# Optimization experiments

Hardware: AMD Instinct MI355X
Metric: run time of the kernel (lower is better)

## Reference

```python
import jax, jax.numpy as jnp
import numpy as np

B, C, H, W = 8, 256, 160, 160

def setup_inputs() -> dict:
    key = jax.random.key(0)
    kx, kw, kh = jax.random.split(key, 3)
    x = jax.random.normal(kx, (B, C, H, W), dtype=jnp.float32)
    # kaiming_normal fan_in, relu -> std = sqrt(2/fan_in)
    fcw_w = jax.random.normal(kw, (1, W), dtype=jnp.float32) * np.float32(np.sqrt(2.0 / W))
    fch_w = jax.random.normal(kh, (1, H), dtype=jnp.float32) * np.float32(np.sqrt(2.0 / H))
    fcw_b = jnp.zeros((1,), dtype=jnp.float32)
    fch_b = jnp.zeros((1,), dtype=jnp.float32)
    return {"x": x, "fcw_w": fcw_w, "fcw_b": fcw_b, "fch_w": fch_w, "fch_b": fch_b}

def reference(x, fcw_w, fcw_b, fch_w, fch_b):
    b, c, h, w = x.shape
    xr = x.reshape(b * c, h, w)                                   # (n,h,w)
    # fc_w: Linear(w,1) then softmax over h (dim=1 of (n,h,1))
    alpha = jax.nn.softmax(jnp.einsum('nhw,w->nh', xr, fcw_w[0]) + fcw_b[0], axis=1)  # (n,h)
    # repeat+bmm == broadcasting a softmax-weighted row-sum to every row:
    # x_c[n,i,:] = sum_h alpha[n,h] * x[n,h,:]  (same for all i)
    row = jnp.einsum('nh,nhw->nw', alpha, xr)                      # (n,w)
    # fc_h on x_c^T (n,w,h): each h-column of x_c^T equals row, so the
    # Linear(h,1) reduces to row * sum(fch_w) + bias (identical math)
    beta = jax.nn.softmax(row * jnp.sum(fch_w[0]) + fch_b[0], axis=1)  # (n,w)
    # second repeat+bmm collapses to a scalar per (b,c): sum_w beta*row
    s = jnp.einsum('nw,nw->n', beta, row)                          # (n,)
    out = jnp.broadcast_to(s[:, None, None], (b * c, h, w)).reshape(b, c, h, w)
    return out
```

## Files before the change

### kernel.cpp

```cpp
#include <hip/hip_runtime.h>


#define HH 160
#define WW 160
#define NPLANE (HH * WW)
#define NPLANES 2048
#define NROWS (NPLANES * HH)

__global__ void __launch_bounds__(256) sa1_logits(
    const float* __restrict__ x,
    const float* __restrict__ fcw_w,
    float* __restrict__ l)
{
    const int wid  = (blockIdx.x * 256 + threadIdx.x) >> 6;
    const int lane = threadIdx.x & 63;

    float4 ww = make_float4(0.f, 0.f, 0.f, 0.f);
    if (lane < 40) ww = *(const float4*)(fcw_w + 4 * lane);

#pragma unroll 4
    for (int k = 0; k < 40; ++k) {
        const int r = wid + (k << 13);
        float p = 0.f;
        if (lane < 40) {
            const float4 xv = *(const float4*)(x + (size_t)r * WW + 4 * lane);
            p = xv.x * ww.x + xv.y * ww.y + xv.z * ww.z + xv.w * ww.w;
        }
#pragma unroll
        for (int off = 32; off >= 1; off >>= 1)
            p += __shfl_xor(p, off, 64);
        if (lane == 0) l[r] = p;
    }
}

__global__ void __launch_bounds__(256) sa1_attn(
    const float* __restrict__ x,
    const float* __restrict__ fch_w,
    const float* __restrict__ l,
    float* __restrict__ s_out)
{
    const int n    = blockIdx.x;
    const int t    = threadIdx.x;
    const int lane = t & 63;
    const int wv   = t >> 6;

    __shared__ float albuf[HH];
    __shared__ float pmax[4], psum[4], pS[4], pzb[4], psd[4];

    float lv = -1e30f, fv = 0.f;
    if (t < HH) { lv = l[n * HH + t]; fv = fch_w[t]; }
    float m = lv, fs = fv;
#pragma unroll
    for (int off = 32; off >= 1; off >>= 1) {
        m  = fmaxf(m, __shfl_xor(m, off, 64));
        fs += __shfl_xor(fs, off, 64);
    }
    if (lane == 0) { pmax[wv] = m; pS[wv] = fs; }
    __syncthreads();
    m = fmaxf(fmaxf(pmax[0], pmax[1]), fmaxf(pmax[2], pmax[3]));
    const float S = pS[0] + pS[1] + pS[2] + pS[3];

    float e = 0.f;
    if (t < HH) { e = __expf(lv - m); albuf[t] = e; }
    float zs = e;
#pragma unroll
    for (int off = 32; off >= 1; off >>= 1)
        zs += __shfl_xor(zs, off, 64);
    if (lane == 0) psum[wv] = zs;
    __syncthreads();
    const float Z = psum[0] + psum[1] + psum[2] + psum[3];

    float acc0 = 0.f, acc1 = 0.f, acc2 = 0.f, acc3 = 0.f;
    if (t < WW) {
        const float* xp = x + (size_t)n * NPLANE + t;
#pragma unroll 4
        for (int h = 0; h < HH; h += 4) {
            acc0 += albuf[h + 0] * xp[(h + 0) * WW];
            acc1 += albuf[h + 1] * xp[(h + 1) * WW];
            acc2 += albuf[h + 2] * xp[(h + 2) * WW];
            acc3 += albuf[h + 3] * xp[(h + 3) * WW];
        }
    }
    const float row = ((acc0 + acc1) + (acc2 + acc3)) / Z;

    float bl = (t < WW) ? row * S : -1e30f;
    float mb = bl;
#pragma unroll
    for (int off = 32; off >= 1; off >>= 1)
        mb = fmaxf(mb, __shfl_xor(mb, off, 64));
    if (lane == 0) pmax[wv] = mb;
    __syncthreads();
    mb = fmaxf(fmaxf(pmax[0], pmax[1]), fmaxf(pmax[2], pmax[3]));

    float e2 = (t < WW) ? __expf(bl - mb) : 0.f;
    float zb = e2, sd = e2 * row;
#pragma unroll
    for (int off = 32; off >= 1; off >>= 1) {
        zb += __shfl_xor(zb, off, 64);
        sd += __shfl_xor(sd, off, 64);
    }
    if (lane == 0) { pzb[wv] = zb; psd[wv] = sd; }
    __syncthreads();
    if (t == 0) {
        const float ZB = pzb[0] + pzb[1] + pzb[2] + pzb[3];
        const float SD = psd[0] + psd[1] + psd[2] + psd[3];
        s_out[n] = SD / ZB;
    }
}

__global__ void __launch_bounds__(256) sa1_bcast(
    const float* __restrict__ s_arr,
    float* __restrict__ out)
{
    const int n = blockIdx.x;
    const int t = threadIdx.x;
    float* op = out + (size_t)n * NPLANE;

    const float sv = s_arr[n];
    const float4 o = make_float4(sv, sv, sv, sv);
#pragma unroll
    for (int k = 0; k < 25; ++k)
        *(float4*)(op + 4 * (size_t)(k * 256 + t)) = o;
}

extern "C" void kernel_launch(void* const* d_in, const int* in_sizes, int n_in,
                              void* d_out, int out_size, void* d_ws, size_t ws_size,
                              hipStream_t stream) {
    const float* x     = (const float*)d_in[0];
    const float* fcw_w = (const float*)d_in[1];
    const float* fch_w = (const float*)d_in[3];
    float* out = (float*)d_out;

    float* l_ws = (float*)d_ws;
    float* s_ws = l_ws + NROWS;

    sa1_logits<<<NPLANES, 256, 0, stream>>>(x, fcw_w, l_ws);
    sa1_attn  <<<NPLANES, 256, 0, stream>>>(x, fch_w, l_ws, s_ws);
    sa1_bcast <<<NPLANES, 256, 0, stream>>>(s_ws, out);
}
```

Measured before the change: 393.6 us.

## Fuse logits and attention into one pass with online softmax

Merges the logits kernel and the attention kernel into a single kernel that reads each plane of x once. Each wave walks every fourth row, computes the row logit, and keeps an online-softmax running max, normaliser and weighted row accumulator. The four per-wave partials are then merged through shared memory. This removes the second full read of x and the intermediate logits buffer, at the cost of extra exp work per row and a serial dependency chain in each wave, with a one-row-ahead prefetch to hide load latency.

```diff
diff --git a/kernel.cpp b/kernel.cpp
--- a/kernel.cpp
+++ b/kernel.cpp
@@ -5,38 +5,11 @@
 #define WW 160
 #define NPLANE (HH * WW)
 #define NPLANES 2048
-#define NROWS (NPLANES * HH)
 
-__global__ void __launch_bounds__(256) sa1_logits(
+__global__ void __launch_bounds__(256, 8) sa1_reduce(
     const float* __restrict__ x,
     const float* __restrict__ fcw_w,
-    float* __restrict__ l)
-{
-    const int wid  = (blockIdx.x * 256 + threadIdx.x) >> 6;
-    const int lane = threadIdx.x & 63;
-
-    float4 ww = make_float4(0.f, 0.f, 0.f, 0.f);
-    if (lane < 40) ww = *(const float4*)(fcw_w + 4 * lane);
-
-#pragma unroll 4
-    for (int k = 0; k < 40; ++k) {
-        const int r = wid + (k << 13);
-        float p = 0.f;
-        if (lane < 40) {
-            const float4 xv = *(const float4*)(x + (size_t)r * WW + 4 * lane);
-            p = xv.x * ww.x + xv.y * ww.y + xv.z * ww.z + xv.w * ww.w;
-        }
-#pragma unroll
-        for (int off = 32; off >= 1; off >>= 1)
-            p += __shfl_xor(p, off, 64);
-        if (lane == 0) l[r] = p;
-    }
-}
-
-__global__ void __launch_bounds__(256) sa1_attn(
-    const float* __restrict__ x,
     const float* __restrict__ fch_w,
-    const float* __restrict__ l,
     float* __restrict__ s_out)
 {
     const int n    = blockIdx.x;
@@ -44,66 +17,85 @@
     const int lane = t & 63;
     const int wv   = t >> 6;
 
-    __shared__ float albuf[HH];
-    __shared__ float pmax[4], psum[4], pS[4], pzb[4], psd[4];
+    __shared__ float racc_s[4 * WW];
+    __shared__ float mzbuf[8];
+    __shared__ float pS[4];
+    __shared__ float red[12];
 
-    float lv = -1e30f, fv = 0.f;
-    if (t < HH) { lv = l[n * HH + t]; fv = fch_w[t]; }
-    float m = lv, fs = fv;
+    float fs = (t < HH) ? fch_w[t] : 0.f;
 #pragma unroll
-    for (int off = 32; off >= 1; off >>= 1) {
-        m  = fmaxf(m, __shfl_xor(m, off, 64));
-        fs += __shfl_xor(fs, off, 64);
+    for (int off = 32; off >= 1; off >>= 1) fs += __shfl_xor(fs, off, 64);
+    if (lane == 0) pS[wv] = fs;
+
+    float4 ww = make_float4(0.f, 0.f, 0.f, 0.f);
+    if (lane < 40) ww = *(const float4*)(fcw_w + 4 * lane);
+
+    const float* xp = x + (size_t)n * NPLANE;
+
+    float  m = -1e30f, Z = 0.f;
+    float4 racc = make_float4(0.f, 0.f, 0.f, 0.f);
+    float4 xv_next = make_float4(0.f, 0.f, 0.f, 0.f);
+    if (lane < 40) xv_next = *(const float4*)(xp + (size_t)wv * WW + 4 * lane);
+
+    for (int r = 0; r < 40; ++r) {
+        const float4 xv = xv_next;
+        if (r < 39 && lane < 40)
+            xv_next = *(const float4*)(xp + (size_t)(wv + 4 * (r + 1)) * WW + 4 * lane);
+
+        float p = (lane < 40)
+                    ? (xv.x * ww.x + xv.y * ww.y + xv.z * ww.z + xv.w * ww.w)
+                    : 0.f;
+#pragma unroll
+        for (int off = 32; off >= 1; off >>= 1) p += __shfl_xor(p, off, 64);
+        const float mn = fmaxf(m, p);
+        const float c  = __expf(m - mn);
+        const float e  = __expf(p - mn);
+        Z = Z * c + e;
+        racc.x = racc.x * c + e * xv.x;
+        racc.y = racc.y * c + e * xv.y;
+        racc.z = racc.z * c + e * xv.z;
+        racc.w = racc.w * c + e * xv.w;
+        m = mn;
     }
-    if (lane == 0) { pmax[wv] = m; pS[wv] = fs; }
+
+    if (lane < 40) *(float4*)(racc_s + wv * WW + 4 * lane) = racc;
+    if (lane == 0) { mzbuf[2 * wv] = m; mzbuf[2 * wv + 1] = Z; }
     __syncthreads();
-    m = fmaxf(fmaxf(pmax[0], pmax[1]), fmaxf(pmax[2], pmax[3]));
+
     const float S = pS[0] + pS[1] + pS[2] + pS[3];
+    const float m0 = mzbuf[0], m1 = mzbuf[2], m2 = mzbuf[4], m3 = mzbuf[6];
+    const float M  = fmaxf(fmaxf(m0, m1), fmaxf(m2, m3));
+    const float s0 = __expf(m0 - M), s1 = __expf(m1 - M);
+    const float s2 = __expf(m2 - M), s3 = __expf(m3 - M);
+    const float Zt = s0 * mzbuf[1] + s1 * mzbuf[3] + s2 * mzbuf[5] + s3 * mzbuf[7];
 
-    float e = 0.f;
-    if (t < HH) { e = __expf(lv - m); albuf[t] = e; }
-    float zs = e;
-#pragma unroll
-    for (int off = 32; off >= 1; off >>= 1)
-        zs += __shfl_xor(zs, off, 64);
-    if (lane == 0) psum[wv] = zs;
-    __syncthreads();
-    const float Z = psum[0] + psum[1] + psum[2] + psum[3];
+    float row = 0.f;
+    if (t < WW) {
+        const float rs = s0 * racc_s[0 * WW + t] + s1 * racc_s[1 * WW + t]
+                       + s2 * racc_s[2 * WW + t] + s3 * racc_s[3 * WW + t];
+        row = rs / Zt;
+    }
 
-    float acc0 = 0.f, acc1 = 0.f, acc2 = 0.f, acc3 = 0.f;
-    if (t < WW) {
-        const float* xp = x + (size_t)n * NPLANE + t;
-#pragma unroll 4
-        for (int h = 0; h < HH; h += 4) {
-            acc0 += albuf[h + 0] * xp[(h + 0) * WW];
-            acc1 += albuf[h + 1] * xp[(h + 1) * WW];
-            acc2 += albuf[h + 2] * xp[(h + 2) * WW];
-            acc3 += albuf[h + 3] * xp[(h + 3) * WW];
-        }
-    }
-    const float row = ((acc0 + acc1) + (acc2 + acc3)) / Z;
-
-    float bl = (t < WW) ? row * S : -1e30f;
+    const float bl = (t < WW) ? row * S : -1e30f;
     float mb = bl;
 #pragma unroll
-    for (int off = 32; off >= 1; off >>= 1)
-        mb = fmaxf(mb, __shfl_xor(mb, off, 64));
-    if (lane == 0) pmax[wv] = mb;
+    for (int off = 32; off >= 1; off >>= 1) mb = fmaxf(mb, __shfl_xor(mb, off, 64));
+    if (lane == 0) red[wv] = mb;
     __syncthreads();
-    mb = fmaxf(fmaxf(pmax[0], pmax[1]), fmaxf(pmax[2], pmax[3]));
+    mb = fmaxf(fmaxf(red[0], red[1]), fmaxf(red[2], red[3]));
 
-    float e2 = (t < WW) ? __expf(bl - mb) : 0.f;
+    const float e2 = (t < WW) ? __expf(bl - mb) : 0.f;
     float zb = e2, sd = e2 * row;
 #pragma unroll
     for (int off = 32; off >= 1; off >>= 1) {
         zb += __shfl_xor(zb, off, 64);
         sd += __shfl_xor(sd, off, 64);
     }
-    if (lane == 0) { pzb[wv] = zb; psd[wv] = sd; }
+    if (lane == 0) { red[4 + wv] = zb; red[8 + wv] = sd; }
     __syncthreads();
     if (t == 0) {
-        const float ZB = pzb[0] + pzb[1] + pzb[2] + pzb[3];
-        const float SD = psd[0] + psd[1] + psd[2] + psd[3];
+        const float ZB = red[4] + red[5] + red[6] + red[7];
+        const float SD = red[8] + red[9] + red[10] + red[11];
         s_out[n] = SD / ZB;
     }
 }
@@ -131,10 +123,8 @@
     const float* fch_w = (const float*)d_in[3];
     float* out = (float*)d_out;
 
-    float* l_ws = (float*)d_ws;
-    float* s_ws = l_ws + NROWS;
+    float* s_ws = (float*)d_ws;
 
-    sa1_logits<<<NPLANES, 256, 0, stream>>>(x, fcw_w, l_ws);
-    sa1_attn  <<<NPLANES, 256, 0, stream>>>(x, fch_w, l_ws, s_ws);
+    sa1_reduce<<<NPLANES, 256, 0, stream>>>(x, fcw_w, fch_w, s_ws);
     sa1_bcast <<<NPLANES, 256, 0, stream>>>(s_ws, out);
 }
```

Measured after the change: 366.9 us. 1.07x faster.
